# Performance work log

Hardware: AMD Instinct MI355X
Metric: run time of the kernel (lower is better)

## Reference

```python
import jax, jax.numpy as jnp
import numpy as np

T, B, D, R, S, M, H = 1024, 4, 1024, 64, 16, 64, 16
NEG_INF = -1e8


def setup_inputs() -> dict:
    key = jax.random.key(0)
    ks = jax.random.split(key, 12)
    Q, K = R + T + S, M + R + T
    inp = {
        "utterance": jax.random.normal(ks[0], (T, B, D), jnp.float32),
        "right_context": jax.random.normal(ks[1], (R, B, D), jnp.float32),
        "summary": jax.random.normal(ks[2], (S, B, D), jnp.float32),
        "mems": jax.random.normal(ks[3], (M, B, D), jnp.float32),
        # valid frame counts in [1, T]; ensure at least one element == T so
        # max(lengths) stresses the full utterance span
        "lengths": jnp.asarray(
            jax.random.randint(ks[4], (B,), 1, T + 1).at[0].set(T), jnp.int32
        ),
        "attention_mask": jax.random.uniform(ks[5], (Q, K)) < 0.1,
        # Linear params stored as (in, out); y = x @ W + b  (== torch Linear)
        "Wq": jax.random.normal(ks[6], (D, D), jnp.float32) * 0.02,
        "bq": jnp.zeros((D,), jnp.float32),
        "Wkv": jax.random.normal(ks[7], (D, 2 * D), jnp.float32) * 0.02,
        "bkv": jnp.zeros((2 * D,), jnp.float32),
        "Wout": jax.random.normal(ks[8], (D, D), jnp.float32) * 0.02,
        "bout": jnp.zeros((D,), jnp.float32),
    }
    return inp


def reference(utterance, right_context, summary, mems, lengths, attention_mask,
              Wq, bq, Wkv, bkv, Wout, bout):
    d_head = D // H
    scaling = d_head ** -0.5
    Q = R + T + S  # query length
    Kl = M + R + T  # key length (non-streaming)

    # projections
    query = jnp.concatenate([right_context, utterance, summary], axis=0) @ Wq + bq  # (Q,B,D)
    kv = jnp.concatenate([mems, right_context, utterance], axis=0) @ Wkv + bkv      # (K,B,2D)
    k, v = jnp.split(kv, 2, axis=2)  # each (K,B,D)

    # (L, B, D) -> (B*H, L, d_head), matching torch view+transpose
    def heads(x):
        return x.reshape(x.shape[0], B * H, d_head).swapaxes(0, 1)

    qh, kh, vh = heads(query), heads(k), heads(v)

    # fp32 scores + masking, as in the original (masked_fill in float)
    w = jnp.einsum("nqd,nkd->nqk", qh * scaling, kh).astype(jnp.float32)  # (B*H,Q,K)
    w = jnp.where(attention_mask[None, :, :], NEG_INF, w)

    # padding mask over keys: klengths = lengths + M + (R+T - max(lengths))
    klengths = lengths + M + R + T - jnp.max(lengths)
    pad = jnp.arange(Kl, dtype=lengths.dtype)[None, :] >= klengths[:, None]  # (B,K)
    w = w.reshape(B, H, Q, Kl)
    w = jnp.where(pad[:, None, None, :], NEG_INF, w)
    w = w.reshape(B * H, Q, Kl)

    probs = jax.nn.softmax(w, axis=-1).astype(utterance.dtype)  # dropout p=0.0

    attn = jnp.einsum("nqk,nkd->nqd", probs, vh)          # (B*H,Q,d)
    attn = attn.swapaxes(0, 1).reshape(Q, B, D)           # (Q,B,D)
    out = attn @ Wout + bout

    output = out[: Q - S]                 # right_context + utterance outputs
    output_mems = jnp.tanh(out[Q - S:])   # summary -> new mems
    out_key = k[M + R:]                   # utterance keys for streaming cache
    out_val = v[M + R:]
    return output, output_mems, out_key, out_val
```

## Files before the change

kernel.cpp:

```cpp
#include <hip/hip_runtime.h>
#include <hip/hip_bf16.h>

typedef __attribute__((ext_vector_type(8))) short short8;
typedef __attribute__((ext_vector_type(4))) float f32x4;

#define DEV __device__ __forceinline__

constexpr int Tn = 1024, Bn = 4, Dn = 1024, Rn = 64, Sn = 16, Mn = 64, Hn = 16;
constexpr int DH = 64;
constexpr int Qn = Rn + Tn + Sn;
constexpr int KL = Mn + Rn + Tn;
constexpr int NT = KL / 64;
constexpr int NQB = 18;
constexpr int QB = Qn * Bn;
constexpr int KB = KL * Bn;
constexpr size_t OUTM = (size_t)(Rn + Tn) * Bn * Dn;
constexpr size_t OUTK = OUTM + (size_t)Sn * Bn * Dn;
constexpr size_t OUTV = OUTK + (size_t)Tn * Bn * Dn;
constexpr size_t NU  = (size_t)Tn * Bn * Dn;
constexpr size_t NR_ = (size_t)Rn * Bn * Dn;
constexpr size_t NS_ = (size_t)Sn * Bn * Dn;
constexpr size_t NM_ = (size_t)Mn * Bn * Dn;
constexpr float QSCALE = 0.18033688f;

DEV float b2f(ushort u) { union { unsigned v; float f; } x; x.v = ((unsigned)u) << 16; return x.f; }
DEV ushort f2b(float f) { __hip_bfloat16 h = __float2bfloat16(f); return *reinterpret_cast<ushort*>(&h); }

DEV float ldbias(const void* p, int i, int fp32) {
    return fp32 ? ((const float*)p)[i] : b2f(((const ushort*)p)[i]);
}
DEV void stout(void* p, size_t i, float v, int fp32) {
    if (fp32) ((float*)p)[i] = v; else ((ushort*)p)[i] = f2b(v);
}
DEV bool mread(const void* m, size_t idx, int mode) {
    if (mode == 0) return ((const unsigned char*)m)[idx] != 0;
    if (mode == 1) return ((const int*)m)[idx] != 0;
    return ((const float*)m)[idx] != 0.f;
}

DEV void gload_lds16(const void* g, void* l) {
    __builtin_amdgcn_global_load_lds(
        (const __attribute__((address_space(1))) unsigned int*)g,
        (__attribute__((address_space(3))) unsigned int*)l, 16, 0, 0);
}

DEV unsigned cvt_pk_bf16(float lo, float hi) {
    unsigned r;
    asm("v_cvt_pk_bf16_f32 %0, %1, %2" : "=v"(r) : "v"(lo), "v"(hi));
    return r;
}

DEV int sigma_key(int v) {
    return (2 * (v >> 5) + ((v & 7) >> 2)) * 16 + ((v >> 3) & 3) * 4 + (v & 3);
}

__global__ __launch_bounds__(256) void probe_kernel(const ushort* utt, const unsigned char* mask,
                                                    int* flags) {
    __shared__ int cnt[4];
    if (threadIdx.x < 4) cnt[threadIdx.x] = 0;
    __syncthreads();
    int c = 0;
    for (int i = threadIdx.x; i < 2048; i += 256) {
        int e = (utt[i] >> 7) & 0xFF;
        if (e > 64 && e < 192) c++;
    }
    atomicAdd(&cnt[0], c);
    int c0 = 0, c1 = 0, c23 = 0;
    for (int i = threadIdx.x; i < 8192; i += 256) {
        if (mask[i]) { int m = i & 3; if (m == 0) c0++; else if (m == 1) c1++; else c23++; }
    }
    atomicAdd(&cnt[1], c0); atomicAdd(&cnt[2], c1); atomicAdd(&cnt[3], c23);
    __syncthreads();
    if (threadIdx.x == 0) {
        flags[0] = (cnt[0] < 1900) ? 1 : 0;
        int mmode;
        if (cnt[2] == 0 && cnt[3] == 0) mmode = 1;
        else if (cnt[1] == 0) mmode = 2;
        else mmode = 0;
        flags[1] = mmode;
    }
}

__global__ __launch_bounds__(256) void build_mbits(const void* __restrict__ amask,
                                                   const int* __restrict__ lengths,
                                                   unsigned long long* __restrict__ mbits,
                                                   const int* __restrict__ flags) {
    const int mmode = flags[1];
    int word = blockIdx.x * 4 + (threadIdx.x >> 6);
    if (word >= Bn * Qn * NT) return;
    int lane = threadIdx.x & 63;
    int ktl = word % NT;
    int rem = word / NT;
    int q = rem % Qn;
    int b = rem / Qn;
    const int l0 = lengths[0], l1 = lengths[1], l2 = lengths[2], l3 = lengths[3];
    const int maxlen = max(max(l0, l1), max(l2, l3));
    const int klen = lengths[b] + KL - maxlen;
    int kg = ktl * 64 + lane;
    bool m = mread(amask, (size_t)q * KL + kg, mmode) || (kg >= klen);
    unsigned long long bal = __ballot(m);
    if (lane == 0) mbits[word] = bal;
}

__global__ __launch_bounds__(256) void convert_acts(const void* utt, const void* rc,
                                                    const void* sm, const void* mm,
                                                    ushort* dst, const int* flags) {
    const int fp32 = flags[0];
    const size_t total = (NU + NR_ + NS_ + NM_) / 8;
    for (size_t cidx = (size_t)blockIdx.x * 256 + threadIdx.x; cidx < total;
         cidx += (size_t)gridDim.x * 256) {
        size_t e = cidx * 8; const void* src; size_t li; ushort* d;
        if (e < NU)                  { src = utt; li = e;                 d = dst; }
        else if (e < NU + NR_)       { src = rc;  li = e - NU;            d = dst + NU; }
        else if (e < NU + NR_ + NS_) { src = sm;  li = e - NU - NR_;      d = dst + NU + NR_; }
        else                         { src = mm;  li = e - NU - NR_ - NS_; d = dst + NU + NR_ + NS_; }
        if (fp32) {
            const float* f = (const float*)src + li;
            ushort o[8];
#pragma unroll
            for (int j = 0; j < 8; ++j) o[j] = f2b(f[j]);
            *(short8*)(d + li) = *(short8*)o;
        } else {
            *(short8*)(d + li) = *(const short8*)((const ushort*)src + li);
        }
    }
}

__global__ __launch_bounds__(256) void transpose_w3(const void* Wq, const void* Wkv, const void* Wout,
                                                    ushort* WqT, ushort* WkvT, ushort* WoutT,
                                                    const int* flags) {
    __shared__ alignas(16) ushort tile[64 * 64];
    const int fp32 = flags[0];
    const int z = blockIdx.z;
    const void* W; ushort* WT; int N;
    int tc = blockIdx.x, tr = blockIdx.y;
    if (z == 0)      { W = Wq;   WT = WqT;   N = 1024; }
    else if (z == 3) { W = Wout; WT = WoutT; N = 1024; }
    else             { W = Wkv;  WT = WkvT;  N = 2048; tc += (z - 1) * 16; }
    const int K = 1024;
    const int t = threadIdx.x;
    for (int c = t; c < 512; c += 256) {
        int row = c >> 3, q = c & 7;
        int u = q ^ (row & 7);
        ushort o[8];
#pragma unroll
        for (int j = 0; j < 8; ++j) {
            size_t gi = (size_t)(tr * 64 + row) * N + tc * 64 + q * 8 + j;
            o[j] = fp32 ? f2b(((const float*)W)[gi]) : ((const ushort*)W)[gi];
        }
        *(short8*)&tile[row * 64 + u * 8] = *(short8*)o;
    }
    __syncthreads();
    for (int c = t; c < 512; c += 256) {
        int n = c >> 3, q = c & 7;
        ushort vv[8];
#pragma unroll
        for (int j = 0; j < 8; ++j) {
            int k = q * 8 + j;
            int u = (n >> 3) ^ (k & 7);
            vv[j] = tile[k * 64 + u * 8 + (n & 7)];
        }
        *(short8*)(WT + (size_t)(tc * 64 + n) * K + tr * 64 + q * 8) = *(short8*)vv;
    }
}

__global__ __launch_bounds__(256) void transpose_v(const ushort* __restrict__ kv,
                                                   ushort* __restrict__ vT) {
    __shared__ alignas(16) ushort tile[64 * 64];
    const int kt = blockIdx.x, bh = blockIdx.y;
    const int b = bh >> 4, h = bh & 15;
    const int t = threadIdx.x;
    for (int c = t; c < 512; c += 256) {
        int key = c >> 3, q = c & 7;
        short8 v = *(const short8*)(kv + ((size_t)(kt * 64 + key) * Bn + b) * 2048 + 1024 + h * DH + q * 8);
        int u = q ^ (key & 7);
        *(short8*)&tile[key * 64 + u * 8] = v;
    }
    __syncthreads();
    for (int c = t; c < 512; c += 256) {
        int d = c >> 3, q = c & 7;
        ushort vv[8];
#pragma unroll
        for (int j = 0; j < 8; ++j) {
            int key = sigma_key(q * 8 + j);
            int u = (d >> 3) ^ (key & 7);
            vv[j] = tile[key * 64 + u * 8 + (d & 7)];
        }
        *(short8*)(vT + ((size_t)bh * 64 + d) * KL + kt * 64 + q * 8) = *(short8*)vv;
    }
}

#define GEMM_STAGE(DSTBUF, KT)                                                        \
    _Pragma("unroll")                                                                 \
    for (int iss = 0; iss < 2; ++iss) {                                               \
        gload_lds16(asrc[iss] + (KT) * 32, &As[DSTBUF][(iss * 256 + w * 64) * 8]);    \
        gload_lds16(bsrc[iss] + (KT) * 32, &Bs[DSTBUF][(iss * 256 + w * 64) * 8]);    \
    }

#define GEMM_PHASE(CUR, PRE, KTN, VMSTR)                                              \
    {                                                                                 \
        if (PRE) { GEMM_STAGE((CUR) ^ 1, KTN); }                                      \
        asm volatile("s_waitcnt " VMSTR ::: "memory");                                \
        __builtin_amdgcn_sched_barrier(0);                                            \
        __builtin_amdgcn_s_barrier();                                                 \
        __builtin_amdgcn_sched_barrier(0);                                            \
        short8 af[4], bfr[4];                                                         \
        _Pragma("unroll")                                                             \
        for (int m = 0; m < 4; ++m) {                                                 \
            int row = wr * 64 + m * 16 + lr;                                          \
            int u = g ^ (row & 3);                                                    \
            af[m] = *(const short8*)&As[CUR][row * 32 + u * 8];                       \
        }                                                                             \
        _Pragma("unroll")                                                             \
        for (int n = 0; n < 4; ++n) {                                                 \
            int col = wc * 64 + n * 16 + lr;                                          \
            int u = g ^ (col & 3);                                                    \
            bfr[n] = *(const short8*)&Bs[CUR][col * 32 + u * 8];                      \
        }                                                                             \
        __builtin_amdgcn_s_setprio(1);                                                \
        _Pragma("unroll")                                                             \
        for (int m = 0; m < 4; ++m)                                                   \
            _Pragma("unroll")                                                         \
            for (int n = 0; n < 4; ++n)                                               \
                acc[m][n] = __builtin_amdgcn_mfma_f32_16x16x32_bf16(af[m], bfr[n], acc[m][n], 0, 0, 0); \
        __builtin_amdgcn_s_setprio(0);                                                \
        __builtin_amdgcn_sched_barrier(0);                                            \
        __builtin_amdgcn_s_barrier();                                                 \
    }

template <int EPI>
__global__ __launch_bounds__(256, 2) void gemm_bt(
    const ushort* __restrict__ A0, const ushort* __restrict__ A1, const ushort* __restrict__ A2,
    int r0, int r1,
    const ushort* __restrict__ Bt, const void* __restrict__ bias,
    int Mrows, int Ncols,
    ushort* __restrict__ C, void* __restrict__ gout, const int* __restrict__ flags) {
    __shared__ alignas(16) ushort As[2][128 * 32];
    __shared__ alignas(16) ushort Bs[2][128 * 32];
    constexpr int Kdim = 1024;
    const int ofp = flags[0];
    const int t = threadIdx.x;
    const int w = t >> 6, lane = t & 63;
    const int wr = w >> 1, wc = w & 1;
    const int g = lane >> 4, lr = lane & 15;

    const int nwg = gridDim.x * gridDim.y;
    const int bid = blockIdx.y * gridDim.x + blockIdx.x;
    const int wg = (bid & 7) * (nwg >> 3) + (bid >> 3);
    const int bx = wg % gridDim.x, by = wg / gridDim.x;
    const int mbase = by * 128, nbase = bx * 128;

    const ushort* asrc[2]; const ushort* bsrc[2];
#pragma unroll
    for (int iss = 0; iss < 2; ++iss) {
        int c = iss * 256 + w * 64 + lane;
        int row = c >> 2, u = c & 3, q = u ^ (row & 3);
        int grow = mbase + row;
        if (grow >= Mrows) grow = Mrows - 1;
        const ushort* s;
        if (grow < r0)      s = A0 + (size_t)grow * Kdim;
        else if (grow < r1) s = A1 + (size_t)(grow - r0) * Kdim;
        else                s = A2 + (size_t)(grow - r1) * Kdim;
        asrc[iss] = s + q * 8;
        bsrc[iss] = Bt + (size_t)(nbase + row) * Kdim + q * 8;
    }

    f32x4 acc[4][4] = {};

    GEMM_STAGE(0, 0);
    for (int k2 = 0; k2 < 30; k2 += 2) {
        GEMM_PHASE(0, true, k2 + 1, "vmcnt(4)");
        GEMM_PHASE(1, true, k2 + 2, "vmcnt(4)");
    }
    GEMM_PHASE(0, true, 31, "vmcnt(4)");
    GEMM_PHASE(1, false, 0, "vmcnt(0)");

#pragma unroll
    for (int n = 0; n < 4; ++n) {
        int col = nbase + wc * 64 + n * 16 + lr;
        float bv = ldbias(bias, col, ofp);
#pragma unroll
        for (int m = 0; m < 4; ++m) {
            int rowb = mbase + wr * 64 + m * 16 + g * 4;
#pragma unroll
            for (int i = 0; i < 4; ++i) {
                int row = rowb + i;
                if (row >= Mrows) continue;
                float val = acc[m][n][i] + bv;
                if (EPI == 0) {
                    C[(size_t)row * Ncols + col] = f2b(val * QSCALE);
                } else if (EPI == 1) {
                    C[(size_t)row * Ncols + col] = f2b(val);
                    if (row >= (Mn + Rn) * Bn) {
                        size_t o = (col < 1024)
                            ? OUTK + (size_t)(row - 512) * 1024 + col
                            : OUTV + (size_t)(row - 512) * 1024 + (col - 1024);
                        stout(gout, o, val, ofp);
                    }
                } else {
                    if (row < (Rn + Tn) * Bn) stout(gout, (size_t)row * 1024 + col, val, ofp);
                    else stout(gout, OUTM + (size_t)(row - (Rn + Tn) * Bn) * 1024 + col, tanhf(val), ofp);
                }
            }
        }
    }
}

#define ATTN_STAGE(DSTBUF, KT)                                                        \
    gload_lds16(ksrc0 + (size_t)(KT) * kstep, &Ks[DSTBUF][w * 1024]);                 \
    gload_lds16(ksrc1 + (size_t)(KT) * kstep, &Ks[DSTBUF][w * 1024 + 512]);           \
    gload_lds16(vsrc0 + (size_t)(KT) * 64,    &Vs[DSTBUF][w * 1024]);                 \
    gload_lds16(vsrc1 + (size_t)(KT) * 64,    &Vs[DSTBUF][w * 1024 + 512]);

#define ATTN_PHASE(CUR, WBCUR, PRE, KTN, WBNXT, VMSTR)                                \
    {                                                                                 \
        if (PRE) { ATTN_STAGE((CUR) ^ 1, KTN); WBNXT = mp[KTN]; }                     \
        asm volatile("s_waitcnt " VMSTR ::: "memory");                                \
        __builtin_amdgcn_sched_barrier(0);                                            \
        __builtin_amdgcn_s_barrier();                                                 \
        __builtin_amdgcn_sched_barrier(0);                                            \
        f32x4 sa[4] = {};                                                             \
        __builtin_amdgcn_s_setprio(1);                                                \
        _Pragma("unroll")                                                             \
        for (int n = 0; n < 4; ++n) {                                                 \
            int key = n * 16 + lr;                                                    \
            short8 kb0 = *(const short8*)&Ks[CUR][key * 64 + ((g ^ (key & 7)) << 3)]; \
            short8 kb1 = *(const short8*)&Ks[CUR][key * 64 + (((4 + g) ^ (key & 7)) << 3)]; \
            sa[n] = __builtin_amdgcn_mfma_f32_16x16x32_bf16(kb0, qf0, sa[n], 0, 0, 0); \
            sa[n] = __builtin_amdgcn_mfma_f32_16x16x32_bf16(kb1, qf1, sa[n], 0, 0, 0); \
        }                                                                             \
        __builtin_amdgcn_s_setprio(0);                                                \
        unsigned pkk[4][2];                                                           \
        _Pragma("unroll")                                                             \
        for (int n = 0; n < 4; ++n) {                                                 \
            unsigned bits = (unsigned)((WBCUR) >> (n * 16 + g * 4)) & 15u;            \
            float p[4];                                                               \
            _Pragma("unroll")                                                         \
            for (int i = 0; i < 4; ++i) {                                             \
                float sv = ((bits >> i) & 1u) ? -100.0f : sa[n][i];                   \
                p[i] = exp2f(sv);                                                     \
                lsum += p[i];                                                         \
            }                                                                         \
            pkk[n][0] = cvt_pk_bf16(p[0], p[1]);                                      \
            pkk[n][1] = cvt_pk_bf16(p[2], p[3]);                                      \
        }                                                                             \
        union { unsigned u[4]; short8 s; } c0, c1;                                    \
        c0.u[0] = pkk[0][0]; c0.u[1] = pkk[0][1]; c0.u[2] = pkk[1][0]; c0.u[3] = pkk[1][1]; \
        c1.u[0] = pkk[2][0]; c1.u[1] = pkk[2][1]; c1.u[2] = pkk[3][0]; c1.u[3] = pkk[3][1]; \
        __builtin_amdgcn_s_setprio(1);                                                \
        _Pragma("unroll")                                                             \
        for (int n = 0; n < 4; ++n) {                                                 \
            int d = n * 16 + lr;                                                      \
            short8 vb0 = *(const short8*)&Vs[CUR][d * 64 + ((g ^ (d & 7)) << 3)];     \
            short8 vb1 = *(const short8*)&Vs[CUR][d * 64 + (((4 + g) ^ (d & 7)) << 3)]; \
            acc_o[n] = __builtin_amdgcn_mfma_f32_16x16x32_bf16(c0.s, vb0, acc_o[n], 0, 0, 0); \
            acc_o[n] = __builtin_amdgcn_mfma_f32_16x16x32_bf16(c1.s, vb1, acc_o[n], 0, 0, 0); \
        }                                                                             \
        __builtin_amdgcn_s_setprio(0);                                                \
        __builtin_amdgcn_sched_barrier(0);                                            \
        __builtin_amdgcn_s_barrier();                                                 \
    }

__global__ __launch_bounds__(256, 5) void attn_kernel(
    const ushort* __restrict__ qws, const ushort* __restrict__ kvws, const ushort* __restrict__ vTws,
    const unsigned long long* __restrict__ mbits,
    ushort* __restrict__ attnws) {
    __shared__ alignas(16) ushort Ks[2][64 * 64];
    __shared__ alignas(16) ushort Vs[2][64 * 64];

    const int bid = blockIdx.x;
    const int wg = (bid & 7) * (gridDim.x >> 3) + (bid >> 3);
    const int qblk = wg % NQB;
    const int bh = wg / NQB;
    const int b = bh >> 4, h = bh & 15;
    const int t = threadIdx.x;
    const int w = t >> 6, lane = t & 63;
    const int g = lane >> 4, lr = lane & 15;

    const int qi = qblk * 64 + w * 16 + lr;
    const int qic = qi < Qn ? qi : (Qn - 1);
    const ushort* qptr = qws + ((size_t)qic * Bn + b) * Dn + h * DH;
    const short8 qf0 = *(const short8*)(qptr + g * 8);
    const short8 qf1 = *(const short8*)(qptr + 32 + g * 8);
    const unsigned long long* mp = mbits + ((size_t)b * Qn + qic) * NT;

    const int srow0 = w * 16 + (lane >> 3);
    const int srow1 = srow0 + 8;
    const int sw = (((lane & 7) ^ ((lane >> 3) & 7)) << 3);
    const ushort* ksrc0 = kvws + ((size_t)srow0 * Bn + b) * 2048 + h * DH + sw;
    const ushort* ksrc1 = kvws + ((size_t)srow1 * Bn + b) * 2048 + h * DH + sw;
    const ushort* vsrc0 = vTws + ((size_t)bh * 64 + srow0) * KL + sw;
    const ushort* vsrc1 = vTws + ((size_t)bh * 64 + srow1) * KL + sw;
    const size_t kstep = (size_t)64 * Bn * 2048;

    f32x4 acc_o[4] = {};
    float lsum = 0.f;
    unsigned long long wbA, wbB;

    ATTN_STAGE(0, 0);
    wbA = mp[0];
    wbB = 0;

    for (int kt2 = 0; kt2 < NT - 2; kt2 += 2) {
        ATTN_PHASE(0, wbA, true, kt2 + 1, wbB, "vmcnt(5)");
        ATTN_PHASE(1, wbB, true, kt2 + 2, wbA, "vmcnt(5)");
    }
    ATTN_PHASE(0, wbA, true, NT - 1, wbB, "vmcnt(5)");
    ATTN_PHASE(1, wbB, false, 0, wbA, "vmcnt(0)");

    float ls = lsum;
    ls += __shfl_xor(ls, 16);
    ls += __shfl_xor(ls, 32);
#pragma unroll
    for (int i = 0; i < 4; ++i) {
        int qrow = g * 4 + i;
        float lsv = __shfl(ls, (lane & 48) | qrow);
        int qg = qblk * 64 + w * 16 + qrow;
        if (qg >= Qn) continue;
        float inv = 1.f / lsv;
#pragma unroll
        for (int n = 0; n < 4; ++n) {
            attnws[((size_t)qg * Bn + b) * Dn + h * DH + n * 16 + lr] = f2b(acc_o[n][i] * inv);
        }
    }
}

extern "C" void kernel_launch(void* const* d_in, const int* in_sizes, int n_in,
                              void* d_out, int out_size, void* d_ws, size_t ws_size,
                              hipStream_t stream) {
    const void* utt   = d_in[0];
    const void* rc    = d_in[1];
    const void* summ  = d_in[2];
    const void* mems  = d_in[3];
    const int*  lens  = (const int*)d_in[4];
    const void* amask = d_in[5];
    const void* Wq   = d_in[6];
    const void* bq   = d_in[7];
    const void* Wkv  = d_in[8];
    const void* bkv  = d_in[9];
    const void* Wout = d_in[10];
    const void* bout = d_in[11];

    ushort* ws    = (ushort*)d_ws;
    int*   flags  = (int*)d_ws;
    ushort* cu    = ws + 64;
    ushort* cutt  = cu;
    ushort* crc   = cutt + NU;
    ushort* csum  = crc + NR_;
    ushort* cmem  = csum + NS_;
    ushort* WqT   = cmem + NM_;
    ushort* WkvT  = WqT + (size_t)1024 * 1024;
    ushort* WoutT = WkvT + (size_t)2048 * 1024;
    ushort* q_ws  = WoutT + (size_t)1024 * 1024;
    ushort* kv_ws = q_ws + (size_t)QB * Dn;
    ushort* vT_ws = kv_ws + (size_t)KB * 2048;
    ushort* at_ws = vT_ws + (size_t)64 * 64 * KL;
    unsigned long long* mbits = (unsigned long long*)(at_ws + (size_t)QB * Dn);

    probe_kernel<<<1, 256, 0, stream>>>((const ushort*)utt, (const unsigned char*)amask, flags);
    build_mbits<<<(Bn * Qn * NT + 3) / 4, 256, 0, stream>>>(amask, lens, mbits, flags);
    convert_acts<<<1024, 256, 0, stream>>>(utt, rc, summ, mems, cu, flags);
    transpose_w3<<<dim3(16, 16, 4), 256, 0, stream>>>(Wq, Wkv, Wout, WqT, WkvT, WoutT, flags);

    gemm_bt<0><<<dim3(8, 35), 256, 0, stream>>>(crc, cutt, csum, Rn * Bn, (Rn + Tn) * Bn,
                                                WqT, bq, QB, 1024, q_ws, nullptr, flags);
    gemm_bt<1><<<dim3(16, 36), 256, 0, stream>>>(cmem, crc, cutt, Mn * Bn, (Mn + Rn) * Bn,
                                                 WkvT, bkv, KB, 2048, kv_ws, d_out, flags);
    transpose_v<<<dim3(KL / 64, Bn * Hn), 256, 0, stream>>>(kv_ws, vT_ws);
    attn_kernel<<<dim3(NQB * Bn * Hn), 256, 0, stream>>>(q_ws, kv_ws, vT_ws, mbits, at_ws);
    gemm_bt<2><<<dim3(8, 35), 256, 0, stream>>>(at_ws, at_ws, at_ws, 0, 0,
                                                WoutT, bout, QB, 1024, nullptr, d_out, flags);
}
```

Baseline: 201.9 us.

## Fuse Q and KV projections into one GEMM and retile output GEMM

```diff
diff --git a/kernel.cpp b/kernel.cpp
--- a/kernel.cpp
+++ b/kernel.cpp
@@ -14,6 +14,7 @@
 constexpr int NQB = 18;
 constexpr int QB = Qn * Bn;
 constexpr int KB = KL * Bn;
+constexpr int MU = 4672;
 constexpr size_t OUTM = (size_t)(Rn + Tn) * Bn * Dn;
 constexpr size_t OUTK = OUTM + (size_t)Sn * Bn * Dn;
 constexpr size_t OUTV = OUTK + (size_t)Tn * Bn * Dn;
@@ -190,33 +191,27 @@
     }
 }
 
-#define GEMM_STAGE(DSTBUF, KT)                                                        \
+#define QKV_STAGE(DSTBUF, KT)                                                         \
     _Pragma("unroll")                                                                 \
     for (int iss = 0; iss < 2; ++iss) {                                               \
         gload_lds16(asrc[iss] + (KT) * 32, &As[DSTBUF][(iss * 256 + w * 64) * 8]);    \
         gload_lds16(bsrc[iss] + (KT) * 32, &Bs[DSTBUF][(iss * 256 + w * 64) * 8]);    \
     }
 
-#define GEMM_PHASE(CUR, PRE, KTN, VMSTR)                                              \
+#define QKV_PHASE(CUR, PRE, KTN, VMSTR)                                               \
     {                                                                                 \
-        if (PRE) { GEMM_STAGE((CUR) ^ 1, KTN); }                                      \
+        if (PRE) { QKV_STAGE((CUR) ^ 1, KTN); }                                       \
         asm volatile("s_waitcnt " VMSTR ::: "memory");                                \
         __builtin_amdgcn_sched_barrier(0);                                            \
         __builtin_amdgcn_s_barrier();                                                 \
         __builtin_amdgcn_sched_barrier(0);                                            \
         short8 af[4], bfr[4];                                                         \
         _Pragma("unroll")                                                             \
-        for (int m = 0; m < 4; ++m) {                                                 \
-            int row = wr * 64 + m * 16 + lr;                                          \
-            int u = g ^ (row & 3);                                                    \
-            af[m] = *(const short8*)&As[CUR][row * 32 + u * 8];                       \
-        }                                                                             \
-        _Pragma("unroll")                                                             \
-        for (int n = 0; n < 4; ++n) {                                                 \
-            int col = wc * 64 + n * 16 + lr;                                          \
-            int u = g ^ (col & 3);                                                    \
-            bfr[n] = *(const short8*)&Bs[CUR][col * 32 + u * 8];                      \
-        }                                                                             \
+        for (int m = 0; m < 4; ++m)                                                   \
+            af[m] = *(const short8*)&As[CUR][(g * 128 + wr * 64 + m * 16 + lr) * 8];  \
+        _Pragma("unroll")                                                             \
+        for (int n = 0; n < 4; ++n)                                                   \
+            bfr[n] = *(const short8*)&Bs[CUR][(g * 128 + wc * 64 + n * 16 + lr) * 8]; \
         __builtin_amdgcn_s_setprio(1);                                                \
         _Pragma("unroll")                                                             \
         for (int m = 0; m < 4; ++m)                                                   \
@@ -228,16 +223,14 @@
         __builtin_amdgcn_s_barrier();                                                 \
     }
 
-template <int EPI>
-__global__ __launch_bounds__(256, 2) void gemm_bt(
-    const ushort* __restrict__ A0, const ushort* __restrict__ A1, const ushort* __restrict__ A2,
-    int r0, int r1,
-    const ushort* __restrict__ Bt, const void* __restrict__ bias,
-    int Mrows, int Ncols,
-    ushort* __restrict__ C, void* __restrict__ gout, const int* __restrict__ flags) {
+__global__ __launch_bounds__(256, 3) void gemm_qkv(
+    const ushort* __restrict__ cmem, const ushort* __restrict__ crc,
+    const ushort* __restrict__ cutt, const ushort* __restrict__ csum,
+    const ushort* __restrict__ Bt, const void* __restrict__ bq, const void* __restrict__ bkv,
+    ushort* __restrict__ q_ws, ushort* __restrict__ kv_ws,
+    void* __restrict__ gout, const int* __restrict__ flags) {
     __shared__ alignas(16) ushort As[2][128 * 32];
     __shared__ alignas(16) ushort Bs[2][128 * 32];
-    constexpr int Kdim = 1024;
     const int ofp = flags[0];
     const int t = threadIdx.x;
     const int w = t >> 6, lane = t & 63;
@@ -253,54 +246,145 @@
     const ushort* asrc[2]; const ushort* bsrc[2];
 #pragma unroll
     for (int iss = 0; iss < 2; ++iss) {
-        int c = iss * 256 + w * 64 + lane;
-        int row = c >> 2, u = c & 3, q = u ^ (row & 3);
+        int tt = w * 64 + lane;
+        int row = tt & 127;
+        int gk = (tt >> 7) + 2 * iss;
         int grow = mbase + row;
-        if (grow >= Mrows) grow = Mrows - 1;
+        if (grow >= MU) grow = MU - 1;
         const ushort* s;
-        if (grow < r0)      s = A0 + (size_t)grow * Kdim;
-        else if (grow < r1) s = A1 + (size_t)(grow - r0) * Kdim;
-        else                s = A2 + (size_t)(grow - r1) * Kdim;
-        asrc[iss] = s + q * 8;
-        bsrc[iss] = Bt + (size_t)(nbase + row) * Kdim + q * 8;
+        if (grow < 256)       s = cmem + (size_t)grow * 1024;
+        else if (grow < 512)  s = crc + (size_t)(grow - 256) * 1024;
+        else if (grow < 4608) s = cutt + (size_t)(grow - 512) * 1024;
+        else                  s = csum + (size_t)(grow - 4608) * 1024;
+        asrc[iss] = s + gk * 8;
+        bsrc[iss] = Bt + (size_t)(nbase + row) * 1024 + gk * 8;
     }
 
     f32x4 acc[4][4] = {};
 
-    GEMM_STAGE(0, 0);
+    QKV_STAGE(0, 0);
     for (int k2 = 0; k2 < 30; k2 += 2) {
-        GEMM_PHASE(0, true, k2 + 1, "vmcnt(4)");
-        GEMM_PHASE(1, true, k2 + 2, "vmcnt(4)");
-    }
-    GEMM_PHASE(0, true, 31, "vmcnt(4)");
-    GEMM_PHASE(1, false, 0, "vmcnt(0)");
+        QKV_PHASE(0, true, k2 + 1, "vmcnt(4)");
+        QKV_PHASE(1, true, k2 + 2, "vmcnt(4)");
+    }
+    QKV_PHASE(0, true, 31, "vmcnt(4)");
+    QKV_PHASE(1, false, 0, "vmcnt(0)");
+
+#pragma unroll
+    for (int n = 0; n < 4; ++n) {
+        int col = nbase + wc * 64 + n * 16 + lr;
+        float bv = (col < 1024) ? ldbias(bq, col, ofp) : ldbias(bkv, col - 1024, ofp);
+#pragma unroll
+        for (int m = 0; m < 4; ++m) {
+            int rowb = mbase + wr * 64 + m * 16 + g * 4;
+#pragma unroll
+            for (int i = 0; i < 4; ++i) {
+                int r = rowb + i;
+                if (r >= MU) continue;
+                float val = acc[m][n][i] + bv;
+                if (col < 1024) {
+                    if (r >= 256) q_ws[(size_t)(r - 256) * 1024 + col] = f2b(val * QSCALE);
+                } else {
+                    if (r < 4608) {
+                        kv_ws[(size_t)r * 2048 + (col - 1024)] = f2b(val);
+                        if (r >= 512) {
+                            size_t o = (col < 2048)
+                                ? OUTK + (size_t)(r - 512) * 1024 + (col - 1024)
+                                : OUTV + (size_t)(r - 512) * 1024 + (col - 2048);
+                            stout(gout, o, val, ofp);
+                        }
+                    }
+                }
+            }
+        }
+    }
+}
+
+#define OUT_STAGE(DSTBUF, KT)                                                         \
+    gload_lds16(asrc + (KT) * 32, &As[DSTBUF][(w * 64) * 8]);                         \
+    _Pragma("unroll")                                                                 \
+    for (int iss = 0; iss < 2; ++iss)                                                 \
+        gload_lds16(bsrc[iss] + (KT) * 32, &Bs[DSTBUF][(iss * 256 + w * 64) * 8]);
+
+#define OUT_PHASE(CUR, PRE, KTN, VMSTR)                                               \
+    {                                                                                 \
+        if (PRE) { OUT_STAGE((CUR) ^ 1, KTN); }                                       \
+        asm volatile("s_waitcnt " VMSTR ::: "memory");                                \
+        __builtin_amdgcn_sched_barrier(0);                                            \
+        __builtin_amdgcn_s_barrier();                                                 \
+        __builtin_amdgcn_sched_barrier(0);                                            \
+        short8 af[2], bfr[4];                                                         \
+        _Pragma("unroll")                                                             \
+        for (int m = 0; m < 2; ++m)                                                   \
+            af[m] = *(const short8*)&As[CUR][(g * 64 + wr * 32 + m * 16 + lr) * 8];   \
+        _Pragma("unroll")                                                             \
+        for (int n = 0; n < 4; ++n)                                                   \
+            bfr[n] = *(const short8*)&Bs[CUR][(g * 128 + wc * 64 + n * 16 + lr) * 8]; \
+        __builtin_amdgcn_s_setprio(1);                                                \
+        _Pragma("unroll")                                                             \
+        for (int m = 0; m < 2; ++m)                                                   \
+            _Pragma("unroll")                                                         \
+            for (int n = 0; n < 4; ++n)                                               \
+                acc[m][n] = __builtin_amdgcn_mfma_f32_16x16x32_bf16(af[m], bfr[n], acc[m][n], 0, 0, 0); \
+        __builtin_amdgcn_s_setprio(0);                                                \
+        __builtin_amdgcn_sched_barrier(0);                                            \
+        __builtin_amdgcn_s_barrier();                                                 \
+    }
+
+__global__ __launch_bounds__(256, 4) void gemm_out(
+    const ushort* __restrict__ A, const ushort* __restrict__ Bt,
+    const void* __restrict__ bias, void* __restrict__ gout, const int* __restrict__ flags) {
+    __shared__ alignas(16) ushort As[2][64 * 32];
+    __shared__ alignas(16) ushort Bs[2][128 * 32];
+    const int ofp = flags[0];
+    const int t = threadIdx.x;
+    const int w = t >> 6, lane = t & 63;
+    const int wr = w >> 1, wc = w & 1;
+    const int g = lane >> 4, lr = lane & 15;
+
+    const int nwg = gridDim.x * gridDim.y;
+    const int bid = blockIdx.y * gridDim.x + blockIdx.x;
+    const int wg = (bid & 7) * (nwg >> 3) + (bid >> 3);
+    const int bx = wg % gridDim.x, by = wg / gridDim.x;
+    const int mbase = by * 64, nbase = bx * 128;
+
+    const ushort* asrc;
+    {
+        int row = t & 63, gk = t >> 6;
+        asrc = A + (size_t)(mbase + row) * 1024 + gk * 8;
+    }
+    const ushort* bsrc[2];
+#pragma unroll
+    for (int iss = 0; iss < 2; ++iss) {
+        int tt = w * 64 + lane;
+        int row = tt & 127;
+        int gk = (tt >> 7) + 2 * iss;
+        bsrc[iss] = Bt + (size_t)(nbase + row) * 1024 + gk * 8;
+    }
+
+    f32x4 acc[2][4] = {};
+
+    OUT_STAGE(0, 0);
+    for (int k2 = 0; k2 < 30; k2 += 2) {
+        OUT_PHASE(0, true, k2 + 1, "vmcnt(3)");
+        OUT_PHASE(1, true, k2 + 2, "vmcnt(3)");
+    }
+    OUT_PHASE(0, true, 31, "vmcnt(3)");
+    OUT_PHASE(1, false, 0, "vmcnt(0)");
 
 #pragma unroll
     for (int n = 0; n < 4; ++n) {
         int col = nbase + wc * 64 + n * 16 + lr;
         float bv = ldbias(bias, col, ofp);
 #pragma unroll
-        for (int m = 0; m < 4; ++m) {
-            int rowb = mbase + wr * 64 + m * 16 + g * 4;
+        for (int m = 0; m < 2; ++m) {
+            int rowb = mbase + wr * 32 + m * 16 + g * 4;
 #pragma unroll
             for (int i = 0; i < 4; ++i) {
                 int row = rowb + i;
-                if (row >= Mrows) continue;
                 float val = acc[m][n][i] + bv;
-                if (EPI == 0) {
-                    C[(size_t)row * Ncols + col] = f2b(val * QSCALE);
-                } else if (EPI == 1) {
-                    C[(size_t)row * Ncols + col] = f2b(val);
-                    if (row >= (Mn + Rn) * Bn) {
-                        size_t o = (col < 1024)
-                            ? OUTK + (size_t)(row - 512) * 1024 + col
-                            : OUTV + (size_t)(row - 512) * 1024 + (col - 1024);
-                        stout(gout, o, val, ofp);
-                    }
-                } else {
-                    if (row < (Rn + Tn) * Bn) stout(gout, (size_t)row * 1024 + col, val, ofp);
-                    else stout(gout, OUTM + (size_t)(row - (Rn + Tn) * Bn) * 1024 + col, tanhf(val), ofp);
-                }
+                if (row < (Rn + Tn) * Bn) stout(gout, (size_t)row * 1024 + col, val, ofp);
+                else stout(gout, OUTM + (size_t)(row - (Rn + Tn) * Bn) * 1024 + col, tanhf(val), ofp);
             }
         }
     }
@@ -462,12 +546,9 @@
     convert_acts<<<1024, 256, 0, stream>>>(utt, rc, summ, mems, cu, flags);
     transpose_w3<<<dim3(16, 16, 4), 256, 0, stream>>>(Wq, Wkv, Wout, WqT, WkvT, WoutT, flags);
 
-    gemm_bt<0><<<dim3(8, 35), 256, 0, stream>>>(crc, cutt, csum, Rn * Bn, (Rn + Tn) * Bn,
-                                                WqT, bq, QB, 1024, q_ws, nullptr, flags);
-    gemm_bt<1><<<dim3(16, 36), 256, 0, stream>>>(cmem, crc, cutt, Mn * Bn, (Mn + Rn) * Bn,
-                                                 WkvT, bkv, KB, 2048, kv_ws, d_out, flags);
+    gemm_qkv<<<dim3(24, 37), 256, 0, stream>>>(cmem, crc, cutt, csum, WqT, bq, bkv,
+                                               q_ws, kv_ws, d_out, flags);
     transpose_v<<<dim3(KL / 64, Bn * Hn), 256, 0, stream>>>(kv_ws, vT_ws);
     attn_kernel<<<dim3(NQB * Bn * Hn), 256, 0, stream>>>(q_ws, kv_ws, vT_ws, mbits, at_ws);
-    gemm_bt<2><<<dim3(8, 35), 256, 0, stream>>>(at_ws, at_ws, at_ws, 0, 0,
-                                                WoutT, bout, QB, 1024, nullptr, d_out, flags);
-}
+    gemm_out<<<dim3(8, 69), 256, 0, stream>>>(at_ws, WoutT, bout, d_out, flags);
+}
```

Result: slower. 229.4 us (+13.6%).
